# Kernel optimization log

Measured on AMD Instinct MI355X. Metric: run time of the kernel, lower is better.

The kernel has to match this reference:

```python
import jax, jax.numpy as jnp
import numpy as np

N = 100000          # nodes
E = 1600000         # edges (avg degree 16)
D_IN = 128
D_OUT = 128
K = 3               # Chebyshev order
LAMBDA_MAX = 2.0    # PyG default for sym normalization


def setup_inputs() -> dict:
    key = jax.random.key(0)
    k1, k2, k3, k4 = jax.random.split(key, 4)
    x = jax.random.normal(k1, (N, D_IN), dtype=jnp.float32)
    edge_index = jax.random.randint(k2, (2, E), 0, N, dtype=jnp.int32)
    # Glorot-ish init for the K per-order linear weights
    weight = jax.random.normal(k3, (K, D_IN, D_OUT), dtype=jnp.float32) * (1.0 / np.sqrt(D_IN))
    bias = jax.random.normal(k4, (D_OUT,), dtype=jnp.float32) * 0.01
    return {"x": x, "edge_index": edge_index, "weight": weight, "bias": bias}


def reference(x, edge_index, weight, bias):
    src, dst = edge_index[0], edge_index[1]
    n = x.shape[0]

    # remove self loops (zero their weight), symmetric normalization
    ew = jnp.where(src != dst, 1.0, 0.0).astype(x.dtype)
    deg = jax.ops.segment_sum(ew, src, num_segments=n)
    dis = jnp.where(deg > 0, jax.lax.rsqrt(jnp.maximum(deg, 1.0)), 0.0)
    norm = dis[src] * ew * dis[dst]          # D^-1/2 A D^-1/2 entries

    # scaled Laplacian T-hat = (2/lmax) L - I, L = I - A_norm
    off_w = -(2.0 / LAMBDA_MAX) * norm       # off-diagonal entries
    diag_w = 2.0 / LAMBDA_MAX - 1.0          # = 0 for lambda_max=2

    def spmm(h):  # T-hat @ h : gather-multiply-scatter over edges
        agg = jax.ops.segment_sum(off_w[:, None] * h[src], dst, num_segments=n)
        return agg + diag_w * h

    # Chebyshev recurrence: Tx_k = 2 T-hat Tx_{k-1} - Tx_{k-2}
    Tx0 = x
    out = Tx0 @ weight[0]
    Tx1 = spmm(Tx0)
    out = out + Tx1 @ weight[1]
    for k in range(2, weight.shape[0]):
        Tx2 = 2.0 * spmm(Tx1) - Tx0
        out = out + Tx2 @ weight[k]
        Tx0, Tx1 = Tx1, Tx2
    return out + bias
```

## Files before the change

kernel.cpp:

```cpp
#include <hip/hip_runtime.h>
#include <hip/hip_bf16.h>

typedef __hip_bfloat16 bf16;
typedef __attribute__((ext_vector_type(8))) short short8;
typedef __attribute__((ext_vector_type(4))) float float4v;
typedef __attribute__((ext_vector_type(2))) float float2v;

#define N_NODES 100000
#define M_PAD   100096
#define N_EDGES 1600000
#define D 128
#define K_CAT 384
#define BUCKET_CAP 56
#define NBIN 392
#define BIN_CAP 4608
#define CHUNK 4096
#define NCHUNK 391
#define PREPB 192
#define QUANTB 25000
#define SPMM_GRID 2048

__device__ __forceinline__ bf16 f2b(float v) { return __float2bfloat16(v); }
__device__ __forceinline__ float ub(unsigned int u, int k) {
    return (float)((u >> (k * 8)) & 0xffu);
}
__device__ __forceinline__ float2v cvt2lo(unsigned int u) {
    float a, b;
    asm("v_cvt_f32_ubyte0 %0, %2\n\t"
        "v_cvt_f32_ubyte1 %1, %2"
        : "=&v"(a), "=&v"(b) : "v"(u));
    float2v o; o.x = a; o.y = b; return o;
}
__device__ __forceinline__ float2v cvt2hi(unsigned int u) {
    float a, b;
    asm("v_cvt_f32_ubyte2 %0, %2\n\t"
        "v_cvt_f32_ubyte3 %1, %2"
        : "=&v"(a), "=&v"(b) : "v"(u));
    float2v o; o.x = a; o.y = b; return o;
}

__global__ __launch_bounds__(256) void phaseA_prep_quant_kernel(
        const int* __restrict__ src, const int* __restrict__ dst,
        const float* __restrict__ w, const float* __restrict__ bias,
        const float* __restrict__ x,
        int* __restrict__ gCursD, int* __restrict__ gCursS,
        unsigned int* __restrict__ gBinD, unsigned char* __restrict__ gBinS,
        bf16* __restrict__ wT, float* __restrict__ biasf,
        unsigned char* __restrict__ xq, float* __restrict__ xscale) {
    __shared__ int histD[NBIN], histS[NBIN], cursD[NBIN], cursS[NBIN];
    int tid = threadIdx.x;
    if (blockIdx.x >= NCHUNK + PREPB) {
        int i = blockIdx.x - (NCHUNK + PREPB);
        int wv = tid >> 6, lane = tid & 63;
        int n = i * 4 + wv;
        float2 v = *(const float2*)(x + (size_t)n * D + lane * 2);
        float m = fmaxf(fabsf(v.x), fabsf(v.y));
#pragma unroll
        for (int k = 1; k < 64; k <<= 1) m = fmaxf(m, __shfl_xor(m, k));
        float inv = (m > 0.0f) ? 127.0f / m : 0.0f;
        int q0 = (int)rintf(v.x * inv) + 128;
        int q1 = (int)rintf(v.y * inv) + 128;
        *(unsigned short*)(xq + (size_t)n * D + lane * 2) =
            (unsigned short)((q0 & 0xff) | ((q1 & 0xff) << 8));
        if (lane == 0) xscale[n] = m * (1.0f / 127.0f);
        return;
    }
    if (blockIdx.x >= NCHUNK) {
        int i = (blockIdx.x - NCHUNK) * 256 + tid;
        int o = i / K_CAT, k = i % K_CAT;
        float v;
        if (k < 128) {
            v = w[k * D + o] - w[2 * 16384 + k * D + o];
        } else if (k < 256) {
            v = w[16384 + (k - 128) * D + o];
        } else {
            v = 2.0f * w[2 * 16384 + (k - 256) * D + o];
        }
        wT[i] = f2b(v);
        if (i < D) biasf[i] = bias[i];
        return;
    }
    for (int t = tid; t < NBIN; t += 256) { histD[t] = 0; histS[t] = 0; }
    __syncthreads();
    int e0 = blockIdx.x * CHUNK;
    for (int i = tid; i < CHUNK; i += 256) {
        int e = e0 + i;
        if (e >= N_EDGES) break;
        int s = src[e], d = dst[e];
        if (s == d) continue;
        atomicAdd(&histD[d >> 8], 1);
        atomicAdd(&histS[s >> 8], 1);
    }
    __syncthreads();
    for (int t = tid; t < NBIN; t += 256) {
        cursD[t] = (histD[t] > 0) ? atomicAdd(&gCursD[t], histD[t]) : 0;
        cursS[t] = (histS[t] > 0) ? atomicAdd(&gCursS[t], histS[t]) : 0;
    }
    __syncthreads();
    for (int i = tid; i < CHUNK; i += 256) {
        int e = e0 + i;
        if (e >= N_EDGES) break;
        int s = src[e], d = dst[e];
        if (s == d) continue;
        int bd = d >> 8, bs = s >> 8;
        int sd = atomicAdd(&cursD[bd], 1);
        if (sd < BIN_CAP) gBinD[(size_t)bd * BIN_CAP + sd] = ((unsigned int)s << 8) | (unsigned int)(d & 255);
        int ss = atomicAdd(&cursS[bs], 1);
        if (ss < BIN_CAP) gBinS[(size_t)bs * BIN_CAP + ss] = (unsigned char)(s & 255);
    }
}

__global__ __launch_bounds__(256) void phaseB_kernel(const int* __restrict__ gCursD,
                                                     const int* __restrict__ gCursS,
                                                     const unsigned int* __restrict__ gBinD,
                                                     const unsigned char* __restrict__ gBinS,
                                                     const float* __restrict__ xscale,
                                                     int* __restrict__ cnt,
                                                     float* __restrict__ dis,
                                                     int* __restrict__ bucket,
                                                     float* __restrict__ dsx0) {
    __shared__ int curs[256];
    int tid = threadIdx.x;
    int b = blockIdx.x;
    curs[tid] = 0;
    __syncthreads();
    if (b < NBIN) {
        int count = min(gCursD[b], BIN_CAP);
        const unsigned int* rec = gBinD + (size_t)b * BIN_CAP;
        int n0 = b << 8;
        for (int j = tid; j < count; j += 256) {
            unsigned int r = rec[j];
            int dloc = r & 255;
            int s = (int)(r >> 8);
            int slot = atomicAdd(&curs[dloc], 1);
            if (slot < BUCKET_CAP) bucket[(size_t)(n0 + dloc) * BUCKET_CAP + slot] = s;
        }
        __syncthreads();
        int n = n0 + tid;
        if (n < N_NODES) cnt[n] = curs[tid];
    } else {
        int bb = b - NBIN;
        int count = min(gCursS[bb], BIN_CAP);
        const unsigned char* rec = gBinS + (size_t)bb * BIN_CAP;
        for (int j = tid; j < count; j += 256) {
            atomicAdd(&curs[rec[j]], 1);
        }
        __syncthreads();
        int n = (bb << 8) + tid;
        if (n < N_NODES) {
            int c = curs[tid];
            float dn = (c > 0) ? rsqrtf((float)c) : 0.0f;
            dis[n] = dn;
            dsx0[n] = dn * xscale[n];
        }
    }
}

template<int OUTQ>
__device__ __forceinline__ void spmm_body(int n,
                                          const unsigned char* __restrict__ hq,
                                          const float* __restrict__ dsx,
                                          const float* __restrict__ dis,
                                          const int* __restrict__ cnt,
                                          const int* __restrict__ bucket,
                                          unsigned char* __restrict__ outq,
                                          float* __restrict__ oscale,
                                          float* __restrict__ odsx,
                                          bf16* __restrict__ outb) {
    int lane = threadIdx.x & 63;
    int c = min(cnt[n], BUCKET_CAP);
    float dn = dis[n];
    int q = lane >> 4;
    int r = lane & 15;
    int s_l = 0;
    float w_l = 0.0f;
    if (lane < c) {
        s_l = bucket[(size_t)n * BUCKET_CAP + lane];
        w_l = -dsx[s_l] * dn;
    }
    const unsigned char* hr = hq + (r << 3);

    float2v acc2[4];
#pragma unroll
    for (int k = 0; k < 4; k++) acc2[k] = (float2v)0.0f;
    float cw = 0.0f;

    int sA = __shfl(s_l, q), sB = __shfl(s_l, 4 + q);
    float wA = __shfl(w_l, q), wB = __shfl(w_l, 4 + q);
    uint2 uA = *(const uint2*)(hr + (size_t)sA * D);
    uint2 uB = *(const uint2*)(hr + (size_t)sB * D);

    for (int j0 = 0; j0 < c; j0 += 8) {
        int nj = j0 + 8;
        int sA2 = __shfl(s_l, nj + q);
        int sB2 = __shfl(s_l, nj + 4 + q);
        float wA2 = __shfl(w_l, nj + q);
        float wB2 = __shfl(w_l, nj + 4 + q);
        uint2 uA2 = *(const uint2*)(hr + (size_t)sA2 * D);
        uint2 uB2 = *(const uint2*)(hr + (size_t)sB2 * D);
        cw += wA + wB;
        float2v wAv; wAv.x = wA; wAv.y = wA;
        float2v wBv; wBv.x = wB; wBv.y = wB;
        acc2[0] += wAv * cvt2lo(uA.x);
        acc2[1] += wAv * cvt2hi(uA.x);
        acc2[2] += wAv * cvt2lo(uA.y);
        acc2[3] += wAv * cvt2hi(uA.y);
        acc2[0] += wBv * cvt2lo(uB.x);
        acc2[1] += wBv * cvt2hi(uB.x);
        acc2[2] += wBv * cvt2lo(uB.y);
        acc2[3] += wBv * cvt2hi(uB.y);
        sA = sA2; sB = sB2; wA = wA2; wB = wB2; uA = uA2; uB = uB2;
    }

    float acc[8];
#pragma unroll
    for (int k = 0; k < 4; k++) { acc[2 * k] = acc2[k].x; acc[2 * k + 1] = acc2[k].y; }
#pragma unroll
    for (int k = 0; k < 8; k++) {
        acc[k] += __shfl_xor(acc[k], 16);
        acc[k] += __shfl_xor(acc[k], 32);
    }
    cw += __shfl_xor(cw, 16);
    cw += __shfl_xor(cw, 32);
#pragma unroll
    for (int k = 0; k < 8; k++) acc[k] -= 128.0f * cw;

    if (OUTQ) {
        float m = 0.0f;
#pragma unroll
        for (int k = 0; k < 8; k++) m = fmaxf(m, fabsf(acc[k]));
#pragma unroll
        for (int k = 1; k < 16; k <<= 1) m = fmaxf(m, __shfl_xor(m, k));
        float inv = (m > 0.0f) ? 127.0f / m : 0.0f;
        if (q == 0) {
            unsigned int b0 = 0, b1 = 0;
#pragma unroll
            for (int k = 0; k < 4; k++)
                b0 |= ((unsigned int)((int)rintf(acc[k] * inv) + 128) & 0xffu) << (8 * k);
#pragma unroll
            for (int k = 0; k < 4; k++)
                b1 |= ((unsigned int)((int)rintf(acc[4 + k] * inv) + 128) & 0xffu) << (8 * k);
            uint2 pk; pk.x = b0; pk.y = b1;
            *(uint2*)(outq + (size_t)n * D + (r << 3)) = pk;
            if (lane == 0) {
                float sc = m * (1.0f / 127.0f);
                oscale[n] = sc;
                odsx[n] = dn * sc;
            }
        }
    } else {
        if (q == 0) {
            unsigned int p0 = (unsigned int)__bfloat16_as_ushort(f2b(acc[0])) |
                              ((unsigned int)__bfloat16_as_ushort(f2b(acc[1])) << 16);
            unsigned int p1 = (unsigned int)__bfloat16_as_ushort(f2b(acc[2])) |
                              ((unsigned int)__bfloat16_as_ushort(f2b(acc[3])) << 16);
            unsigned int p2 = (unsigned int)__bfloat16_as_ushort(f2b(acc[4])) |
                              ((unsigned int)__bfloat16_as_ushort(f2b(acc[5])) << 16);
            unsigned int p3 = (unsigned int)__bfloat16_as_ushort(f2b(acc[6])) |
                              ((unsigned int)__bfloat16_as_ushort(f2b(acc[7])) << 16);
            uint4 pk; pk.x = p0; pk.y = p1; pk.z = p2; pk.w = p3;
            *(uint4*)(outb + (size_t)n * D + (r << 3)) = pk;
        }
    }
}

template<int OUTQ>
__global__ __launch_bounds__(256) void spmm_q_kernel(const unsigned char* __restrict__ hq,
                                                     const float* __restrict__ dsx,
                                                     const float* __restrict__ dis,
                                                     const int* __restrict__ cnt,
                                                     const int* __restrict__ bucket,
                                                     unsigned char* __restrict__ outq,
                                                     float* __restrict__ oscale,
                                                     float* __restrict__ odsx,
                                                     bf16* __restrict__ outb) {
    int wv = threadIdx.x >> 6;
    for (int g = blockIdx.x; g < N_NODES / 4; g += gridDim.x)
        spmm_body<OUTQ>(g * 4 + wv, hq, dsx, dis, cnt, bucket, outq, oscale, odsx, outb);
}

#define AS_STRIDE 40
__device__ __forceinline__ void stage_q8(bf16* __restrict__ As,
                                         const unsigned char* __restrict__ srcq,
                                         const float* __restrict__ scl,
                                         int nb, int kb) {
    int tid = threadIdx.x;
#pragma unroll
    for (int t = 0; t < 2; t++) {
        int c = tid + t * 256;
        int row = c >> 2;
        int off = (c & 3) * 8;
        int gr = nb + row;
        if (gr > N_NODES - 1) gr = N_NODES - 1;
        uint2 u = *(const uint2*)(srcq + (size_t)gr * D + kb + off);
        float sc = scl[gr];
        float f0 = sc * (ub(u.x, 0) - 128.0f);
        float f1 = sc * (ub(u.x, 1) - 128.0f);
        float f2 = sc * (ub(u.x, 2) - 128.0f);
        float f3 = sc * (ub(u.x, 3) - 128.0f);
        float f4 = sc * (ub(u.y, 0) - 128.0f);
        float f5 = sc * (ub(u.y, 1) - 128.0f);
        float f6 = sc * (ub(u.y, 2) - 128.0f);
        float f7 = sc * (ub(u.y, 3) - 128.0f);
        uint4 pk;
        pk.x = (unsigned int)__bfloat16_as_ushort(f2b(f0)) |
               ((unsigned int)__bfloat16_as_ushort(f2b(f1)) << 16);
        pk.y = (unsigned int)__bfloat16_as_ushort(f2b(f2)) |
               ((unsigned int)__bfloat16_as_ushort(f2b(f3)) << 16);
        pk.z = (unsigned int)__bfloat16_as_ushort(f2b(f4)) |
               ((unsigned int)__bfloat16_as_ushort(f2b(f5)) << 16);
        pk.w = (unsigned int)__bfloat16_as_ushort(f2b(f6)) |
               ((unsigned int)__bfloat16_as_ushort(f2b(f7)) << 16);
        *(uint4*)(As + row * AS_STRIDE + off) = pk;
    }
}

__global__ __launch_bounds__(256) void gemm_kernel(const unsigned char* __restrict__ xq,
                                                   const float* __restrict__ xscale,
                                                   const unsigned char* __restrict__ tx1q,
                                                   const float* __restrict__ tx1scale,
                                                   const bf16* __restrict__ agg2,
                                                   const bf16* __restrict__ wT,
                                                   const float* __restrict__ biasf,
                                                   float* __restrict__ out) {
    __shared__ bf16 As[128 * AS_STRIDE];
    __shared__ bf16 Bs[128 * AS_STRIDE];

    int tid = threadIdx.x;
    int nb = blockIdx.x * 128;
    int w = tid >> 6;
    int lane = tid & 63;
    int lq = lane >> 4;
    int lr = lane & 15;

    float4v acc[2][8];
#pragma unroll
    for (int i = 0; i < 2; i++)
#pragma unroll
        for (int j = 0; j < 8; j++) acc[i][j] = (float4v)0.0f;

    for (int kc = 0; kc < 12; kc++) {
        int kbase = kc * 32;
        if (kc < 4) {
            stage_q8(As, xq, xscale, nb, kc * 32);
        } else if (kc < 8) {
            stage_q8(As, tx1q, tx1scale, nb, (kc - 4) * 32);
        } else {
            int soff = (kc & 3) * 32;
#pragma unroll
            for (int t = 0; t < 2; t++) {
                int c = tid + t * 256;
                int row = c >> 2;
                int off = (c & 3) * 8;
                uint4 v = *(const uint4*)(agg2 + (size_t)(nb + row) * D + soff + off);
                *(uint4*)(As + row * AS_STRIDE + off) = v;
            }
        }
#pragma unroll
        for (int t = 0; t < 2; t++) {
            int c = tid + t * 256;
            int row = c >> 2;
            int off = (c & 3) * 8;
            uint4 v = *(const uint4*)(wT + (size_t)row * K_CAT + kbase + off);
            *(uint4*)(Bs + row * AS_STRIDE + off) = v;
        }
        __syncthreads();

        short8 af[2], bfr[8];
#pragma unroll
        for (int i = 0; i < 2; i++)
            af[i] = *(const short8*)(As + (w * 32 + i * 16 + lr) * AS_STRIDE + lq * 8);
#pragma unroll
        for (int j = 0; j < 8; j++)
            bfr[j] = *(const short8*)(Bs + (j * 16 + lr) * AS_STRIDE + lq * 8);
#pragma unroll
        for (int i = 0; i < 2; i++)
#pragma unroll
            for (int j = 0; j < 8; j++)
                acc[i][j] = __builtin_amdgcn_mfma_f32_16x16x32_bf16(af[i], bfr[j], acc[i][j], 0, 0, 0);
        __syncthreads();
    }

#pragma unroll
    for (int i = 0; i < 2; i++) {
        int rowb = nb + w * 32 + i * 16 + lq * 4;
#pragma unroll
        for (int j = 0; j < 8; j++) {
            int col = j * 16 + lr;
            float bv = biasf[col];
#pragma unroll
            for (int r = 0; r < 4; r++) {
                int row = rowb + r;
                if (row < N_NODES) out[(size_t)row * D + col] = acc[i][j][r] + bv;
            }
        }
    }
}

extern "C" void kernel_launch(void* const* d_in, const int* in_sizes, int n_in,
                              void* d_out, int out_size, void* d_ws, size_t ws_size,
                              hipStream_t stream) {
    const float* x    = (const float*)d_in[0];
    const int*   ei   = (const int*)d_in[1];
    const float* w    = (const float*)d_in[2];
    const float* bias = (const float*)d_in[3];
    float* out = (float*)d_out;

    char* p = (char*)d_ws;
    int*   cnt      = (int*)p;     p += (size_t)N_NODES * 4;
    float* dis      = (float*)p;   p += (size_t)N_NODES * 4;
    int*   gCurs    = (int*)p;     p += (size_t)2 * NBIN * 4;
    float* dsx0     = (float*)p;   p += (size_t)M_PAD * 4;
    float* xscale   = (float*)p;   p += (size_t)M_PAD * 4;
    float* tx1scale = (float*)p;   p += (size_t)M_PAD * 4;
    float* dsx1     = (float*)p;   p += (size_t)M_PAD * 4;
    int*   bucket   = (int*)p;     p += (size_t)N_NODES * BUCKET_CAP * 4;
    char*  buf1     = p;           p += (size_t)M_PAD * D;
    unsigned char* xq = (unsigned char*)p; p += (size_t)M_PAD * D;
    bf16*  agg2     = (bf16*)p;    p += (size_t)M_PAD * D * 2;
    bf16*  wT       = (bf16*)p;    p += (size_t)D * K_CAT * 2;
    float* biasf    = (float*)p;   p += (size_t)D * 4;

    int*   gCursD = gCurs;
    int*   gCursS = gCurs + NBIN;
    unsigned int*  gBinD = (unsigned int*)buf1;
    unsigned char* gBinS = (unsigned char*)(gBinD + (size_t)NBIN * BIN_CAP);
    unsigned char* tx1q  = (unsigned char*)buf1;

    hipMemsetAsync(gCurs, 0, (size_t)2 * NBIN * 4, stream);

    phaseA_prep_quant_kernel<<<NCHUNK + PREPB + QUANTB, 256, 0, stream>>>(
        ei, ei + N_EDGES, w, bias, x,
        gCursD, gCursS, gBinD, gBinS, wT, biasf, xq, xscale);
    phaseB_kernel<<<2 * NBIN, 256, 0, stream>>>(gCursD, gCursS, gBinD, gBinS, xscale,
                                                cnt, dis, bucket, dsx0);
    spmm_q_kernel<1><<<SPMM_GRID, 256, 0, stream>>>(xq, dsx0, dis, cnt, bucket,
                                                    tx1q, tx1scale, dsx1, (bf16*)nullptr);
    spmm_q_kernel<0><<<SPMM_GRID, 256, 0, stream>>>(tx1q, dsx1, dis, cnt, bucket,
                                                    (unsigned char*)nullptr, (float*)nullptr,
                                                    (float*)nullptr, agg2);
    gemm_kernel<<<M_PAD / 128, 256, 0, stream>>>(xq, xscale, tx1q, tx1scale,
                                                 agg2, wT, biasf, out);
}
```

Before: 316.8 us.

## Fuse second SpMM into GEMM kernel, keeping aggregated rows in shared memory

The second Chebyshev SpMM is folded into the final GEMM kernel. Each 512-thread block first aggregates its 128 rows into a bf16 shared-memory tile, then runs the concatenated-K MFMA GEMM using that tile for the last third of K. This removes one kernel launch and the global write and read of the bf16 agg2 intermediate. In exchange, the GEMM block now serializes the gather phase before the MMA loop, uses more LDS per block (lowering occupancy), and launches only about 782 blocks for the gather work instead of a 2048-block grid.

```diff
diff --git a/kernel.cpp b/kernel.cpp
--- a/kernel.cpp
+++ b/kernel.cpp
@@ -19,6 +19,7 @@
 #define PREPB 192
 #define QUANTB 25000
 #define SPMM_GRID 2048
+#define AS_STRIDE 40
 
 __device__ __forceinline__ bf16 f2b(float v) { return __float2bfloat16(v); }
 __device__ __forceinline__ float ub(unsigned int u, int k) {
@@ -156,20 +157,12 @@
     }
 }
 
-template<int OUTQ>
-__device__ __forceinline__ void spmm_body(int n,
-                                          const unsigned char* __restrict__ hq,
-                                          const float* __restrict__ dsx,
-                                          const float* __restrict__ dis,
-                                          const int* __restrict__ cnt,
-                                          const int* __restrict__ bucket,
-                                          unsigned char* __restrict__ outq,
-                                          float* __restrict__ oscale,
-                                          float* __restrict__ odsx,
-                                          bf16* __restrict__ outb) {
+__device__ __forceinline__ void spmm_acc(int n, int c, float dn,
+                                         const unsigned char* __restrict__ hq,
+                                         const float* __restrict__ dsx,
+                                         const int* __restrict__ bucket,
+                                         float acc[8]) {
     int lane = threadIdx.x & 63;
-    int c = min(cnt[n], BUCKET_CAP);
-    float dn = dis[n];
     int q = lane >> 4;
     int r = lane & 15;
     int s_l = 0;
@@ -212,7 +205,6 @@
         sA = sA2; sB = sB2; wA = wA2; wB = wB2; uA = uA2; uB = uB2;
     }
 
-    float acc[8];
 #pragma unroll
     for (int k = 0; k < 4; k++) { acc[2 * k] = acc2[k].x; acc[2 * k + 1] = acc2[k].y; }
 #pragma unroll
@@ -224,8 +216,25 @@
     cw += __shfl_xor(cw, 32);
 #pragma unroll
     for (int k = 0; k < 8; k++) acc[k] -= 128.0f * cw;
-
-    if (OUTQ) {
+}
+
+__global__ __launch_bounds__(256) void spmm_q_kernel(const unsigned char* __restrict__ hq,
+                                                     const float* __restrict__ dsx,
+                                                     const float* __restrict__ dis,
+                                                     const int* __restrict__ cnt,
+                                                     const int* __restrict__ bucket,
+                                                     unsigned char* __restrict__ outq,
+                                                     float* __restrict__ oscale,
+                                                     float* __restrict__ odsx) {
+    int wv = threadIdx.x >> 6;
+    int lane = threadIdx.x & 63;
+    int q = lane >> 4, r = lane & 15;
+    for (int g = blockIdx.x; g < N_NODES / 4; g += gridDim.x) {
+        int n = g * 4 + wv;
+        int c = min(cnt[n], BUCKET_CAP);
+        float dn = dis[n];
+        float acc[8];
+        spmm_acc(n, c, dn, hq, dsx, bucket, acc);
         float m = 0.0f;
 #pragma unroll
         for (int k = 0; k < 8; k++) m = fmaxf(m, fabsf(acc[k]));
@@ -248,151 +257,119 @@
                 odsx[n] = dn * sc;
             }
         }
-    } else {
-        if (q == 0) {
-            unsigned int p0 = (unsigned int)__bfloat16_as_ushort(f2b(acc[0])) |
-                              ((unsigned int)__bfloat16_as_ushort(f2b(acc[1])) << 16);
-            unsigned int p1 = (unsigned int)__bfloat16_as_ushort(f2b(acc[2])) |
-                              ((unsigned int)__bfloat16_as_ushort(f2b(acc[3])) << 16);
-            unsigned int p2 = (unsigned int)__bfloat16_as_ushort(f2b(acc[4])) |
-                              ((unsigned int)__bfloat16_as_ushort(f2b(acc[5])) << 16);
-            unsigned int p3 = (unsigned int)__bfloat16_as_ushort(f2b(acc[6])) |
-                              ((unsigned int)__bfloat16_as_ushort(f2b(acc[7])) << 16);
-            uint4 pk; pk.x = p0; pk.y = p1; pk.z = p2; pk.w = p3;
-            *(uint4*)(outb + (size_t)n * D + (r << 3)) = pk;
-        }
-    }
-}
-
-template<int OUTQ>
-__global__ __launch_bounds__(256) void spmm_q_kernel(const unsigned char* __restrict__ hq,
-                                                     const float* __restrict__ dsx,
-                                                     const float* __restrict__ dis,
-                                                     const int* __restrict__ cnt,
-                                                     const int* __restrict__ bucket,
-                                                     unsigned char* __restrict__ outq,
-                                                     float* __restrict__ oscale,
-                                                     float* __restrict__ odsx,
-                                                     bf16* __restrict__ outb) {
-    int wv = threadIdx.x >> 6;
-    for (int g = blockIdx.x; g < N_NODES / 4; g += gridDim.x)
-        spmm_body<OUTQ>(g * 4 + wv, hq, dsx, dis, cnt, bucket, outq, oscale, odsx, outb);
-}
-
-#define AS_STRIDE 40
-__device__ __forceinline__ void stage_q8(bf16* __restrict__ As,
-                                         const unsigned char* __restrict__ srcq,
-                                         const float* __restrict__ scl,
-                                         int nb, int kb) {
-    int tid = threadIdx.x;
-#pragma unroll
-    for (int t = 0; t < 2; t++) {
-        int c = tid + t * 256;
-        int row = c >> 2;
-        int off = (c & 3) * 8;
-        int gr = nb + row;
-        if (gr > N_NODES - 1) gr = N_NODES - 1;
-        uint2 u = *(const uint2*)(srcq + (size_t)gr * D + kb + off);
-        float sc = scl[gr];
-        float f0 = sc * (ub(u.x, 0) - 128.0f);
-        float f1 = sc * (ub(u.x, 1) - 128.0f);
-        float f2 = sc * (ub(u.x, 2) - 128.0f);
-        float f3 = sc * (ub(u.x, 3) - 128.0f);
-        float f4 = sc * (ub(u.y, 0) - 128.0f);
-        float f5 = sc * (ub(u.y, 1) - 128.0f);
-        float f6 = sc * (ub(u.y, 2) - 128.0f);
-        float f7 = sc * (ub(u.y, 3) - 128.0f);
-        uint4 pk;
-        pk.x = (unsigned int)__bfloat16_as_ushort(f2b(f0)) |
-               ((unsigned int)__bfloat16_as_ushort(f2b(f1)) << 16);
-        pk.y = (unsigned int)__bfloat16_as_ushort(f2b(f2)) |
-               ((unsigned int)__bfloat16_as_ushort(f2b(f3)) << 16);
-        pk.z = (unsigned int)__bfloat16_as_ushort(f2b(f4)) |
-               ((unsigned int)__bfloat16_as_ushort(f2b(f5)) << 16);
-        pk.w = (unsigned int)__bfloat16_as_ushort(f2b(f6)) |
-               ((unsigned int)__bfloat16_as_ushort(f2b(f7)) << 16);
-        *(uint4*)(As + row * AS_STRIDE + off) = pk;
-    }
-}
-
-__global__ __launch_bounds__(256) void gemm_kernel(const unsigned char* __restrict__ xq,
-                                                   const float* __restrict__ xscale,
-                                                   const unsigned char* __restrict__ tx1q,
-                                                   const float* __restrict__ tx1scale,
-                                                   const bf16* __restrict__ agg2,
-                                                   const bf16* __restrict__ wT,
-                                                   const float* __restrict__ biasf,
-                                                   float* __restrict__ out) {
+    }
+}
+
+__global__ __launch_bounds__(512) void spmm2_gemm_kernel(
+        const unsigned char* __restrict__ tx1q,
+        const float* __restrict__ dsx1,
+        const float* __restrict__ dis,
+        const int* __restrict__ cnt,
+        const int* __restrict__ bucket,
+        const unsigned char* __restrict__ xq,
+        const float* __restrict__ xscale,
+        const float* __restrict__ tx1scale,
+        const bf16* __restrict__ wT,
+        const float* __restrict__ biasf,
+        float* __restrict__ out) {
     __shared__ bf16 As[128 * AS_STRIDE];
     __shared__ bf16 Bs[128 * AS_STRIDE];
+    __shared__ bf16 aggS[4][128 * AS_STRIDE];
 
     int tid = threadIdx.x;
-    int nb = blockIdx.x * 128;
     int w = tid >> 6;
     int lane = tid & 63;
     int lq = lane >> 4;
     int lr = lane & 15;
-
-    float4v acc[2][8];
-#pragma unroll
-    for (int i = 0; i < 2; i++)
-#pragma unroll
-        for (int j = 0; j < 8; j++) acc[i][j] = (float4v)0.0f;
+    int nb = blockIdx.x * 128;
+
+    for (int t = 0; t < 16; t++) {
+        int nloc = w * 16 + t;
+        int n = nb + nloc;
+        int c = 0;
+        float dn = 0.0f;
+        if (n < N_NODES) { c = min(cnt[n], BUCKET_CAP); dn = dis[n]; }
+        float acc[8];
+        spmm_acc(n, c, dn, tx1q, dsx1, bucket, acc);
+        if (lq == 0) {
+            uint4 pk;
+            pk.x = (unsigned int)__bfloat16_as_ushort(f2b(acc[0])) |
+                   ((unsigned int)__bfloat16_as_ushort(f2b(acc[1])) << 16);
+            pk.y = (unsigned int)__bfloat16_as_ushort(f2b(acc[2])) |
+                   ((unsigned int)__bfloat16_as_ushort(f2b(acc[3])) << 16);
+            pk.z = (unsigned int)__bfloat16_as_ushort(f2b(acc[4])) |
+                   ((unsigned int)__bfloat16_as_ushort(f2b(acc[5])) << 16);
+            pk.w = (unsigned int)__bfloat16_as_ushort(f2b(acc[6])) |
+                   ((unsigned int)__bfloat16_as_ushort(f2b(acc[7])) << 16);
+            *(uint4*)(&aggS[lr >> 2][nloc * AS_STRIDE + (lr & 3) * 8]) = pk;
+        }
+    }
+    __syncthreads();
+
+    float4v acc[8];
+#pragma unroll
+    for (int j = 0; j < 8; j++) acc[j] = (float4v)0.0f;
 
     for (int kc = 0; kc < 12; kc++) {
         int kbase = kc * 32;
-        if (kc < 4) {
-            stage_q8(As, xq, xscale, nb, kc * 32);
-        } else if (kc < 8) {
-            stage_q8(As, tx1q, tx1scale, nb, (kc - 4) * 32);
-        } else {
-            int soff = (kc & 3) * 32;
-#pragma unroll
-            for (int t = 0; t < 2; t++) {
-                int c = tid + t * 256;
-                int row = c >> 2;
-                int off = (c & 3) * 8;
-                uint4 v = *(const uint4*)(agg2 + (size_t)(nb + row) * D + soff + off);
-                *(uint4*)(As + row * AS_STRIDE + off) = v;
-            }
-        }
-#pragma unroll
-        for (int t = 0; t < 2; t++) {
-            int c = tid + t * 256;
-            int row = c >> 2;
-            int off = (c & 3) * 8;
+        if (kc < 8) {
+            const unsigned char* srcq = (kc < 4) ? xq : tx1q;
+            const float* scl = (kc < 4) ? xscale : tx1scale;
+            int kb = (kc & 3) * 32;
+            int row = tid >> 2;
+            int off = (tid & 3) * 8;
+            int gr = nb + row;
+            if (gr > N_NODES - 1) gr = N_NODES - 1;
+            uint2 u = *(const uint2*)(srcq + (size_t)gr * D + kb + off);
+            float sc = scl[gr];
+            float f0 = sc * (ub(u.x, 0) - 128.0f);
+            float f1 = sc * (ub(u.x, 1) - 128.0f);
+            float f2 = sc * (ub(u.x, 2) - 128.0f);
+            float f3 = sc * (ub(u.x, 3) - 128.0f);
+            float f4 = sc * (ub(u.y, 0) - 128.0f);
+            float f5 = sc * (ub(u.y, 1) - 128.0f);
+            float f6 = sc * (ub(u.y, 2) - 128.0f);
+            float f7 = sc * (ub(u.y, 3) - 128.0f);
+            uint4 pk;
+            pk.x = (unsigned int)__bfloat16_as_ushort(f2b(f0)) |
+                   ((unsigned int)__bfloat16_as_ushort(f2b(f1)) << 16);
+            pk.y = (unsigned int)__bfloat16_as_ushort(f2b(f2)) |
+                   ((unsigned int)__bfloat16_as_ushort(f2b(f3)) << 16);
+            pk.z = (unsigned int)__bfloat16_as_ushort(f2b(f4)) |
+                   ((unsigned int)__bfloat16_as_ushort(f2b(f5)) << 16);
+            pk.w = (unsigned int)__bfloat16_as_ushort(f2b(f6)) |
+                   ((unsigned int)__bfloat16_as_ushort(f2b(f7)) << 16);
+            *(uint4*)(As + row * AS_STRIDE + off) = pk;
+        }
+        {
+            int row = tid >> 2;
+            int off = (tid & 3) * 8;
             uint4 v = *(const uint4*)(wT + (size_t)row * K_CAT + kbase + off);
             *(uint4*)(Bs + row * AS_STRIDE + off) = v;
         }
         __syncthreads();
 
-        short8 af[2], bfr[8];
-#pragma unroll
-        for (int i = 0; i < 2; i++)
-            af[i] = *(const short8*)(As + (w * 32 + i * 16 + lr) * AS_STRIDE + lq * 8);
+        const bf16* Asrc = (kc < 8) ? As : aggS[kc - 8];
+        short8 af = *(const short8*)(Asrc + (w * 16 + lr) * AS_STRIDE + lq * 8);
+        short8 bfr[8];
 #pragma unroll
         for (int j = 0; j < 8; j++)
             bfr[j] = *(const short8*)(Bs + (j * 16 + lr) * AS_STRIDE + lq * 8);
 #pragma unroll
-        for (int i = 0; i < 2; i++)
-#pragma unroll
-            for (int j = 0; j < 8; j++)
-                acc[i][j] = __builtin_amdgcn_mfma_f32_16x16x32_bf16(af[i], bfr[j], acc[i][j], 0, 0, 0);
+        for (int j = 0; j < 8; j++)
+            acc[j] = __builtin_amdgcn_mfma_f32_16x16x32_bf16(af, bfr[j], acc[j], 0, 0, 0);
         __syncthreads();
     }
 
-#pragma unroll
-    for (int i = 0; i < 2; i++) {
-        int rowb = nb + w * 32 + i * 16 + lq * 4;
-#pragma unroll
-        for (int j = 0; j < 8; j++) {
-            int col = j * 16 + lr;
-            float bv = biasf[col];
-#pragma unroll
-            for (int r = 0; r < 4; r++) {
-                int row = rowb + r;
-                if (row < N_NODES) out[(size_t)row * D + col] = acc[i][j][r] + bv;
-            }
+    int rowb = nb + w * 16 + lq * 4;
+#pragma unroll
+    for (int j = 0; j < 8; j++) {
+        int col = j * 16 + lr;
+        float bv = biasf[col];
+#pragma unroll
+        for (int r = 0; r < 4; r++) {
+            int row = rowb + r;
+            if (row < N_NODES) out[(size_t)row * D + col] = acc[j][r] + bv;
         }
     }
 }
@@ -417,7 +394,6 @@
     int*   bucket   = (int*)p;     p += (size_t)N_NODES * BUCKET_CAP * 4;
     char*  buf1     = p;           p += (size_t)M_PAD * D;
     unsigned char* xq = (unsigned char*)p; p += (size_t)M_PAD * D;
-    bf16*  agg2     = (bf16*)p;    p += (size_t)M_PAD * D * 2;
     bf16*  wT       = (bf16*)p;    p += (size_t)D * K_CAT * 2;
     float* biasf    = (float*)p;   p += (size_t)D * 4;
 
@@ -434,11 +410,9 @@
         gCursD, gCursS, gBinD, gBinS, wT, biasf, xq, xscale);
     phaseB_kernel<<<2 * NBIN, 256, 0, stream>>>(gCursD, gCursS, gBinD, gBinS, xscale,
                                                 cnt, dis, bucket, dsx0);
-    spmm_q_kernel<1><<<SPMM_GRID, 256, 0, stream>>>(xq, dsx0, dis, cnt, bucket,
-                                                    tx1q, tx1scale, dsx1, (bf16*)nullptr);
-    spmm_q_kernel<0><<<SPMM_GRID, 256, 0, stream>>>(tx1q, dsx1, dis, cnt, bucket,
-                                                    (unsigned char*)nullptr, (float*)nullptr,
-                                                    (float*)nullptr, agg2);
-    gemm_kernel<<<M_PAD / 128, 256, 0, stream>>>(xq, xscale, tx1q, tx1scale,
-                                                 agg2, wT, biasf, out);
-}
+    spmm_q_kernel<<<SPMM_GRID, 256, 0, stream>>>(xq, dsx0, dis, cnt, bucket,
+                                                 tx1q, tx1scale, dsx1);
+    spmm2_gemm_kernel<<<M_PAD / 128, 512, 0, stream>>>(tx1q, dsx1, dis, cnt, bucket,
+                                                       xq, xscale, tx1scale,
+                                                       wT, biasf, out);
+}
```

Result: slower. 339.3 us (+7.1%).
